# Optimization experiments

Hardware: AMD Instinct MI355X
Metric: run time of the kernel (lower is better)

Reference implementation:

```python
import jax, jax.numpy as jnp
import numpy as np

V, C, D, H, L = 32000, 1024, 768, 12, 6
B, S = 2, 1024
HD = D // H
EPS = 1e-5


def _layernorm(x, g, b):
    m = jnp.mean(x, axis=-1, keepdims=True)
    v = jnp.mean((x - m) ** 2, axis=-1, keepdims=True)
    return (x - m) * jax.lax.rsqrt(v + EPS) * g + b


def setup_inputs() -> dict:
    key = jax.random.key(0)
    ks = jax.random.split(key, 20)
    p = lambda k, *sh: (jax.random.normal(k, sh, dtype=jnp.float32) * 0.02)
    inp = {
        'context': jax.random.randint(ks[0], (B, S), 0, V, dtype=jnp.int32),
        'tok_emb': p(ks[1], V, D),
        'pos_emb': p(ks[2], C, D),
        # per-layer stacked params (leading dim L)
        'Wq': p(ks[3], L, D, D), 'Wk': p(ks[4], L, D, D), 'Wv': p(ks[5], L, D, D),
        'Wo': p(ks[6], L, D, D), 'bo': jnp.zeros((L, D), jnp.float32),
        'ln1_g': jnp.ones((L, D), jnp.float32), 'ln1_b': jnp.zeros((L, D), jnp.float32),
        'W1': p(ks[7], L, D, 4 * D), 'b1': jnp.zeros((L, 4 * D), jnp.float32),
        'W2': p(ks[8], L, 4 * D, D), 'b2': jnp.zeros((L, D), jnp.float32),
        'ln2_g': jnp.ones((L, D), jnp.float32), 'ln2_b': jnp.zeros((L, D), jnp.float32),
        'lnf_g': jnp.ones((D,), jnp.float32), 'lnf_b': jnp.zeros((D,), jnp.float32),
        'Wout': p(ks[9], D, V), 'bout': jnp.zeros((V,), jnp.float32),
    }
    return inp


def _forward(context, tok_emb, pos_emb, Wq, Wk, Wv, Wo, bo, ln1_g, ln1_b,
             W1, b1, W2, b2, ln2_g, ln2_b, lnf_g, lnf_b, Wout, bout):
    x = tok_emb[context] + pos_emb[:S]              # [B,S,D]
    causal = jnp.tril(jnp.ones((S, S), dtype=bool))  # [S,S]
    scale = 1.0 / float(HD) ** 0.5

    def step(x, params):
        wq, wk, wv, wo, bo_, g1, b1_, w1, bf1, w2, bf2, g2, b2_ = params
        h = _layernorm(x, g1, b1_)
        q = (h @ wq).reshape(B, S, H, HD)
        k = (h @ wk).reshape(B, S, H, HD)
        v = (h @ wv).reshape(B, S, H, HD)
        scores = jnp.einsum('bqhd,bkhd->bhqk', q, k) * scale
        scores = jnp.where(causal, scores, -jnp.inf)
        attn = jax.nn.softmax(scores, axis=-1)
        ctx = jnp.einsum('bhqk,bkhd->bqhd', attn, v).reshape(B, S, D)
        x = x + ctx @ wo + bo_  # dropout is eval-mode identity
        h2 = _layernorm(x, g2, b2_)
        x = x + jax.nn.relu(h2 @ w1 + bf1) @ w2 + bf2
        return x, None

    params = (Wq, Wk, Wv, Wo, bo, ln1_g, ln1_b, W1, b1, W2, b2, ln2_g, ln2_b)
    x, _ = jax.lax.scan(step, x, params)
    return _layernorm(x, lnf_g, lnf_b) @ Wout + bout  # [B,S,V]


def reference(context, tok_emb, pos_emb, Wq, Wk, Wv, Wo, bo, ln1_g, ln1_b,
              W1, b1, W2, b2, ln2_g, ln2_b, lnf_g, lnf_b, Wout, bout):
    return _forward(context, tok_emb, pos_emb, Wq, Wk, Wv, Wo, bo, ln1_g, ln1_b,
                    W1, b1, W2, b2, ln2_g, ln2_b, lnf_g, lnf_b, Wout, bout)
```

## Files before the change

### kernel.cpp

```cpp
#include <hip/hip_runtime.h>

#define S_    1024
#define D_    768
#define H_    12
#define HD_   64
#define L_    6
#define B_    2
#define V_    32000
#define NTOK  2048
#define DD    (D_ * D_)
#define D4D   (D_ * 4 * D_)

typedef __bf16 bf16_t;
typedef __bf16 bf16x8 __attribute__((ext_vector_type(8)));
typedef float  f32x4  __attribute__((ext_vector_type(4)));

__device__ __forceinline__ void async_ld16(const bf16_t* g, bf16_t* l) {
  __builtin_amdgcn_global_load_lds((__attribute__((address_space(1))) void*)(g),
                                   (__attribute__((address_space(3))) void*)(l),
                                   16, 0, 0);
}

__device__ __forceinline__ float wave_sum(float v) {
#pragma unroll
  for (int off = 32; off; off >>= 1) v += __shfl_xor(v, off);
  return v;
}
__device__ __forceinline__ float wave_max(float v) {
#pragma unroll
  for (int off = 32; off; off >>= 1) v = fmaxf(v, __shfl_xor(v, off));
  return v;
}

__device__ __forceinline__ float ldv(const void* p, size_t i, bool f32) {
  return f32 ? ((const float*)p)[i] : (float)((const bf16_t*)p)[i];
}

__global__ void k_sniff(const void* tok, int* flag) {
  const bf16_t* p = (const bf16_t*)tok;
  float mx = 0.f;
  for (int i = threadIdx.x; i < 256; i += 64) {
    float v = fabsf((float)p[i]);
    mx = fmaxf(mx, v);
  }
  mx = wave_max(mx);
  if (threadIdx.x == 0) *flag = (mx > 1.0e6f) ? 1 : 0;
}

__global__ __launch_bounds__(256) void k_cvt_bias(const int* flag, bf16_t* canon,
    const void* bo, const void* b1, const void* b2, const void* l1g, const void* l1b,
    const void* l2g, const void* l2b, const void* lfg, const void* lfb, const void* bout) {
  const bool f32 = (*flag != 0);
  const void* src; int off, n;
  switch (blockIdx.y) {
    case 0: src = bo;  off = 0;     n = 4608;  break;
    case 1: src = b1;  off = 4608;  n = 18432; break;
    case 2: src = b2;  off = 23040; n = 4608;  break;
    case 3: src = l1g; off = 27648; n = 4608;  break;
    case 4: src = l1b; off = 32256; n = 4608;  break;
    case 5: src = l2g; off = 36864; n = 4608;  break;
    case 6: src = l2b; off = 41472; n = 4608;  break;
    case 7: src = lfg; off = 46080; n = 768;   break;
    case 8: src = lfb; off = 46848; n = 768;   break;
    default: src = bout; off = 47616; n = 32000; break;
  }
  const int i = blockIdx.x * 256 + threadIdx.x;
  if (i < n) canon[off + i] = (bf16_t)ldv(src, (size_t)i, f32);
}

enum { E_STORE = 0, E_BIAS_OUT = 1, E_BIAS_RELU = 2, E_BIAS_RES = 3 };

template <int EPI>
__device__ __forceinline__ void gemm_core(const bf16_t* __restrict__ A,
                                          const bf16_t* __restrict__ BT,
                                          const bf16_t* __restrict__ bias,
                                          void* __restrict__ Cb,
                                          float* __restrict__ resid,
                                          const int* f32out,
                                          int M, int N, int K) {
  __shared__ bf16_t sA[128 * 32];
  __shared__ bf16_t sB[128 * 32];
  const int tid  = threadIdx.x;
  const int wave = tid >> 6, lane = tid & 63;
  const int quad = lane >> 4, l16 = lane & 15;
  const int m0 = blockIdx.y * 128, n0 = blockIdx.x * 128;
  const int wm = (wave >> 1) * 64, wn = (wave & 1) * 64;

  const f32x4 zero = {0.f, 0.f, 0.f, 0.f};
  f32x4 acc[4][4];
#pragma unroll
  for (int i = 0; i < 4; i++)
#pragma unroll
    for (int j = 0; j < 4; j++) acc[i][j] = zero;

  const bf16_t* gA = A  + (size_t)(m0 + wave * 32 + (lane >> 2)) * K + (lane & 3) * 8;
  const bf16_t* gB = BT + (size_t)(n0 + wave * 32 + (lane >> 2)) * K + (lane & 3) * 8;
  bf16_t* lA = sA + wave * 1024;
  bf16_t* lB = sB + wave * 1024;
  const size_t k16 = (size_t)16 * K;

  for (int k0 = 0; k0 < K; k0 += 32) {
    async_ld16(gA, lA);
    async_ld16(gA + k16, lA + 512);
    async_ld16(gB, lB);
    async_ld16(gB + k16, lB + 512);
    gA += 32; gB += 32;
    __syncthreads();

    bf16x8 af[4], bfr[4];
#pragma unroll
    for (int i = 0; i < 4; i++) {
      af[i]  = *(const bf16x8*)(sA + (wm + i * 16 + l16) * 32 + quad * 8);
      bfr[i] = *(const bf16x8*)(sB + (wn + i * 16 + l16) * 32 + quad * 8);
    }
#pragma unroll
    for (int mi = 0; mi < 4; mi++)
#pragma unroll
      for (int ni = 0; ni < 4; ni++)
        acc[mi][ni] = __builtin_amdgcn_mfma_f32_16x16x32_bf16(af[mi], bfr[ni], acc[mi][ni], 0, 0, 0);
    __syncthreads();
  }

  const bool f32o = (EPI == E_BIAS_OUT) && (*f32out != 0);
#pragma unroll
  for (int mi = 0; mi < 4; mi++) {
#pragma unroll
    for (int ni = 0; ni < 4; ni++) {
      const int r0 = m0 + wm + mi * 16 + quad * 4;
      const int c  = n0 + wn + ni * 16 + l16;
      float bv = 0.f;
      if (EPI != E_STORE) bv = (float)bias[c];
#pragma unroll
      for (int r = 0; r < 4; r++) {
        float val = acc[mi][ni][r] + bv;
        if (EPI == E_BIAS_RELU) val = fmaxf(val, 0.f);
        const size_t idx = (size_t)(r0 + r) * N + c;
        if (EPI == E_BIAS_RES) {
          resid[idx] += val;
        } else if (EPI == E_BIAS_OUT) {
          if (f32o) ((float*)Cb)[idx] = val;
          else      ((bf16_t*)Cb)[idx] = (bf16_t)val;
        } else {
          ((bf16_t*)Cb)[idx] = (bf16_t)val;
        }
      }
    }
  }
}

__global__ __launch_bounds__(256) void k_gemm_qkv(const bf16_t* __restrict__ A,
                                                  const bf16_t* __restrict__ BT0,
                                                  const bf16_t* __restrict__ BT1,
                                                  const bf16_t* __restrict__ BT2,
                                                  bf16_t* __restrict__ o0,
                                                  bf16_t* __restrict__ o1,
                                                  bf16_t* __restrict__ o2,
                                                  int M, int N, int K) {
  const bf16_t* BT = (blockIdx.z == 0) ? BT0 : (blockIdx.z == 1) ? BT1 : BT2;
  bf16_t* o = (blockIdx.z == 0) ? o0 : (blockIdx.z == 1) ? o1 : o2;
  gemm_core<E_STORE>(A, BT, nullptr, o, nullptr, nullptr, M, N, K);
}
__global__ __launch_bounds__(256) void k_gemm_bias_relu(const bf16_t* __restrict__ A, const bf16_t* __restrict__ BT,
                                                        const bf16_t* __restrict__ bias, bf16_t* __restrict__ C,
                                                        int M, int N, int K) {
  gemm_core<E_BIAS_RELU>(A, BT, bias, C, nullptr, nullptr, M, N, K);
}
__global__ __launch_bounds__(256) void k_gemm_bias_res(const bf16_t* __restrict__ A, const bf16_t* __restrict__ BT,
                                                       const bf16_t* __restrict__ bias, float* __restrict__ resid,
                                                       int M, int N, int K) {
  gemm_core<E_BIAS_RES>(A, BT, bias, nullptr, resid, nullptr, M, N, K);
}
__global__ __launch_bounds__(256) void k_gemm_out(const bf16_t* __restrict__ A, const bf16_t* __restrict__ BT,
                                                  const bf16_t* __restrict__ bias, void* __restrict__ C,
                                                  const int* flag, int M, int N, int K) {
  gemm_core<E_BIAS_OUT>(A, BT, bias, C, nullptr, flag, M, N, K);
}

__global__ __launch_bounds__(256) void k_t(const int* flag, const void* __restrict__ in, size_t eoff,
                                           bf16_t* __restrict__ out, int K, int N) {
  __shared__ bf16_t t[32][33];
  const bool f32 = (*flag != 0);
  const int n0 = blockIdx.x * 32, k0 = blockIdx.y * 32;
  const int tx = threadIdx.x, ty = threadIdx.y;
#pragma unroll
  for (int i = 0; i < 4; i++)
    t[ty + 8 * i][tx] = (bf16_t)ldv(in, eoff + (size_t)(k0 + ty + 8 * i) * N + n0 + tx, f32);
  __syncthreads();
#pragma unroll
  for (int i = 0; i < 4; i++)
    out[(size_t)(n0 + ty + 8 * i) * K + k0 + tx] = t[tx][ty + 8 * i];
}

__global__ __launch_bounds__(256) void k_t_qkv(const int* flag, const void* __restrict__ Wq,
                                               const void* __restrict__ Wk, const void* __restrict__ Wv,
                                               size_t eoff, bf16_t* __restrict__ out) {
  __shared__ bf16_t t[32][33];
  const bool f32 = (*flag != 0);
  const void* in = (blockIdx.z == 0) ? Wq : (blockIdx.z == 1) ? Wk : Wv;
  bf16_t* o = out + (size_t)blockIdx.z * DD;
  const int n0 = blockIdx.x * 32, k0 = blockIdx.y * 32;
  const int tx = threadIdx.x, ty = threadIdx.y;
#pragma unroll
  for (int i = 0; i < 4; i++)
    t[ty + 8 * i][tx] = (bf16_t)ldv(in, eoff + (size_t)(k0 + ty + 8 * i) * D_ + n0 + tx, f32);
  __syncthreads();
#pragma unroll
  for (int i = 0; i < 4; i++)
    o[(size_t)(n0 + ty + 8 * i) * D_ + k0 + tx] = t[tx][ty + 8 * i];
}

__global__ __launch_bounds__(256) void k_vt(const bf16_t* __restrict__ v, bf16_t* __restrict__ vt) {
  __shared__ bf16_t t[32][33];
  const int b = blockIdx.z;
  const int n0 = blockIdx.x * 32, s0 = blockIdx.y * 32;
  const int tx = threadIdx.x, ty = threadIdx.y;
#pragma unroll
  for (int i = 0; i < 4; i++)
    t[ty + 8 * i][tx] = v[(size_t)(b * S_ + s0 + ty + 8 * i) * D_ + n0 + tx];
  __syncthreads();
#pragma unroll
  for (int i = 0; i < 4; i++)
    vt[(size_t)(b * D_ + n0 + ty + 8 * i) * S_ + s0 + tx] = t[tx][ty + 8 * i];
}

__global__ __launch_bounds__(256) void k_embed(const int* flag, const int* __restrict__ cidx,
                                               const void* __restrict__ tok, const void* __restrict__ pos,
                                               float* __restrict__ x) {
  const bool f32 = (*flag != 0);
  const int t = blockIdx.x;
  const int id = cidx[t];
  const int s = t & (S_ - 1);
  for (int d = threadIdx.x; d < D_; d += 256)
    x[(size_t)t * D_ + d] = ldv(tok, (size_t)id * D_ + d, f32) + ldv(pos, (size_t)s * D_ + d, f32);
}

__global__ __launch_bounds__(256) void k_ln(const float* __restrict__ x, const bf16_t* __restrict__ g,
                                            const bf16_t* __restrict__ bta, bf16_t* __restrict__ out) {
  __shared__ float red[4];
  const int t = blockIdx.x, tid = threadIdx.x;
  const int wave = tid >> 6, lane = tid & 63;
  const float* xr = x + (size_t)t * D_;
  const float v0 = xr[tid], v1 = xr[tid + 256], v2 = xr[tid + 512];
  float s = wave_sum(v0 + v1 + v2);
  if (lane == 0) red[wave] = s;
  __syncthreads();
  const float mean = (red[0] + red[1] + red[2] + red[3]) * (1.f / 768.f);
  const float d0 = v0 - mean, d1 = v1 - mean, d2 = v2 - mean;
  float vs = wave_sum(d0 * d0 + d1 * d1 + d2 * d2);
  __syncthreads();
  if (lane == 0) red[wave] = vs;
  __syncthreads();
  const float inv = rsqrtf((red[0] + red[1] + red[2] + red[3]) * (1.f / 768.f) + 1e-5f);
  bf16_t* o = out + (size_t)t * D_;
  o[tid]       = (bf16_t)(d0 * inv * (float)g[tid]       + (float)bta[tid]);
  o[tid + 256] = (bf16_t)(d1 * inv * (float)g[tid + 256] + (float)bta[tid + 256]);
  o[tid + 512] = (bf16_t)(d2 * inv * (float)g[tid + 512] + (float)bta[tid + 512]);
}

__global__ __launch_bounds__(64) void k_fattn(const bf16_t* __restrict__ q,
                                              const bf16_t* __restrict__ k,
                                              const bf16_t* __restrict__ vt,
                                              bf16_t* __restrict__ ctx) {
  __shared__ bf16_t sP[16 * 40];
  const int lane = threadIdx.x;
  const int quad = lane >> 4, l16 = lane & 15;
  const int q0 = blockIdx.x << 4, h = blockIdx.y, b = blockIdx.z;
  const size_t hoff = (size_t)h * HD_;

  const bf16_t* qp = q + (size_t)(b * S_ + q0 + l16) * D_ + hoff + quad * 8;
  const bf16x8 af0 = *(const bf16x8*)qp;
  const bf16x8 af1 = *(const bf16x8*)(qp + 32);

  const f32x4 zero = {0.f, 0.f, 0.f, 0.f};
  f32x4 o_acc[4];
  float m_run[4], l_run[4];
#pragma unroll
  for (int ct = 0; ct < 4; ++ct) o_acc[ct] = zero;
#pragma unroll
  for (int r = 0; r < 4; ++r) { m_run[r] = -1e30f; l_run[r] = 0.f; }

  const int nt = ((q0 + 15) >> 5) + 1;
  const bf16_t* kbase = k + (size_t)(b * S_ + l16) * D_ + hoff + quad * 8;
  const size_t kst = (size_t)16 * D_;
  bf16x8 kf0 = *(const bf16x8*)(kbase);
  bf16x8 kf1 = *(const bf16x8*)(kbase + 32);
  bf16x8 kf2 = *(const bf16x8*)(kbase + kst);
  bf16x8 kf3 = *(const bf16x8*)(kbase + kst + 32);

  const bf16_t* vbase = vt + (size_t)(b * D_ + hoff + l16) * S_ + quad * 8;

  for (int kt = 0; kt < nt; ++kt) {
    const int k0 = kt << 5;
    const bf16_t* vrow = vbase + k0;
    const bf16x8 vb0 = *(const bf16x8*)(vrow);
    const bf16x8 vb1 = *(const bf16x8*)(vrow + 16 * S_);
    const bf16x8 vb2 = *(const bf16x8*)(vrow + 32 * S_);
    const bf16x8 vb3 = *(const bf16x8*)(vrow + 48 * S_);

    f32x4 d0 = zero, d1 = zero;
    d0 = __builtin_amdgcn_mfma_f32_16x16x32_bf16(af0, kf0, d0, 0, 0, 0);
    d0 = __builtin_amdgcn_mfma_f32_16x16x32_bf16(af1, kf1, d0, 0, 0, 0);
    d1 = __builtin_amdgcn_mfma_f32_16x16x32_bf16(af0, kf2, d1, 0, 0, 0);
    d1 = __builtin_amdgcn_mfma_f32_16x16x32_bf16(af1, kf3, d1, 0, 0, 0);

    if (kt + 1 < nt) {
      const bf16_t* kpn = kbase + (size_t)(k0 + 32) * D_;
      kf0 = *(const bf16x8*)(kpn);
      kf1 = *(const bf16x8*)(kpn + 32);
      kf2 = *(const bf16x8*)(kpn + kst);
      kf3 = *(const bf16x8*)(kpn + kst + 32);
    }

    const bool msk = (kt == nt - 1);
    float al[4];
#pragma unroll
    for (int r = 0; r < 4; ++r) {
      float s0 = d0[r] * 0.125f;
      float s1 = d1[r] * 0.125f;
      if (msk) {
        const int row = q0 + quad * 4 + r;
        if (k0 + l16      > row) s0 = -1e30f;
        if (k0 + 16 + l16 > row) s1 = -1e30f;
      }
      float mt = fmaxf(s0, s1);
      mt = fmaxf(mt, __shfl_xor(mt, 1));
      mt = fmaxf(mt, __shfl_xor(mt, 2));
      mt = fmaxf(mt, __shfl_xor(mt, 4));
      mt = fmaxf(mt, __shfl_xor(mt, 8));
      const float mn = fmaxf(m_run[r], mt);
      const float a  = __expf(m_run[r] - mn);
      m_run[r] = mn;
      const float p0 = __expf(s0 - mn);
      const float p1 = __expf(s1 - mn);
      float ps = p0 + p1;
      ps += __shfl_xor(ps, 1);
      ps += __shfl_xor(ps, 2);
      ps += __shfl_xor(ps, 4);
      ps += __shfl_xor(ps, 8);
      l_run[r] = l_run[r] * a + ps;
      al[r] = a;
      sP[(quad * 4 + r) * 40 + l16]      = (bf16_t)p0;
      sP[(quad * 4 + r) * 40 + 16 + l16] = (bf16_t)p1;
    }
#pragma unroll
    for (int ct = 0; ct < 4; ++ct) {
      o_acc[ct][0] *= al[0]; o_acc[ct][1] *= al[1];
      o_acc[ct][2] *= al[2]; o_acc[ct][3] *= al[3];
    }
    const bf16x8 pa = *(const bf16x8*)(sP + l16 * 40 + quad * 8);
    o_acc[0] = __builtin_amdgcn_mfma_f32_16x16x32_bf16(pa, vb0, o_acc[0], 0, 0, 0);
    o_acc[1] = __builtin_amdgcn_mfma_f32_16x16x32_bf16(pa, vb1, o_acc[1], 0, 0, 0);
    o_acc[2] = __builtin_amdgcn_mfma_f32_16x16x32_bf16(pa, vb2, o_acc[2], 0, 0, 0);
    o_acc[3] = __builtin_amdgcn_mfma_f32_16x16x32_bf16(pa, vb3, o_acc[3], 0, 0, 0);
  }

  float inv[4];
#pragma unroll
  for (int r = 0; r < 4; ++r) inv[r] = 1.f / l_run[r];
  bf16_t* cp = ctx + (size_t)(b * S_ + q0 + quad * 4) * D_ + hoff + l16;
#pragma unroll
  for (int ct = 0; ct < 4; ++ct)
#pragma unroll
    for (int r = 0; r < 4; ++r)
      cp[(size_t)r * D_ + ct * 16] = (bf16_t)(o_acc[ct][r] * inv[r]);
}

extern "C" void kernel_launch(void* const* d_in, const int* in_sizes, int n_in,
                              void* d_out, int out_size, void* d_ws, size_t ws_size,
                              hipStream_t stream) {
  (void)in_sizes; (void)n_in; (void)out_size; (void)ws_size;
  const int* cidx = (const int*)d_in[0];
  const void* tok  = d_in[1];
  const void* pos  = d_in[2];
  const void* Wq   = d_in[3];
  const void* Wk   = d_in[4];
  const void* Wv   = d_in[5];
  const void* Wo   = d_in[6];
  const void* bo   = d_in[7];
  const void* ln1g = d_in[8];
  const void* ln1b = d_in[9];
  const void* W1   = d_in[10];
  const void* b1   = d_in[11];
  const void* W2   = d_in[12];
  const void* b2   = d_in[13];
  const void* ln2g = d_in[14];
  const void* ln2b = d_in[15];
  const void* lnfg = d_in[16];
  const void* lnfb = d_in[17];
  const void* Wout = d_in[18];
  const void* bout = d_in[19];

  char* p = (char*)d_ws;
  int*    flag  = (int*)p;
  bf16_t* canon = (bf16_t*)(p + 256);
  char*   q     = p + 256 + 163840;
  float*  x     = (float*)q;  q += (size_t)NTOK * D_ * 4;
  bf16_t* h     = (bf16_t*)q; q += (size_t)NTOK * D_ * 2;
  bf16_t* qb    = (bf16_t*)q; q += (size_t)NTOK * D_ * 2;
  bf16_t* kbuf  = (bf16_t*)q; q += (size_t)NTOK * D_ * 2;
  bf16_t* vbuf  = (bf16_t*)q; q += (size_t)NTOK * D_ * 2;
  bf16_t* cbuf  = (bf16_t*)q; q += (size_t)NTOK * D_ * 2;
  bf16_t* mid   = (bf16_t*)q; q += (size_t)NTOK * 4 * D_ * 2;
  bf16_t* slot  = (bf16_t*)q; q += (size_t)D_ * V_ * 2;
  bf16_t* vt = mid;

  bf16_t* c_bo  = canon + 0;
  bf16_t* c_b1  = canon + 4608;
  bf16_t* c_b2  = canon + 23040;
  bf16_t* c_l1g = canon + 27648;
  bf16_t* c_l1b = canon + 32256;
  bf16_t* c_l2g = canon + 36864;
  bf16_t* c_l2b = canon + 41472;
  bf16_t* c_lfg = canon + 46080;
  bf16_t* c_lfb = canon + 46848;
  bf16_t* c_bout= canon + 47616;

  const dim3 tb(32, 8);
  k_sniff<<<1, 64, 0, stream>>>(tok, flag);
  k_cvt_bias<<<dim3(125, 10), 256, 0, stream>>>(flag, canon, bo, b1, b2, ln1g, ln1b,
                                                ln2g, ln2b, lnfg, lnfb, bout);
  k_embed<<<NTOK, 256, 0, stream>>>(flag, cidx, tok, pos, x);

  const dim3 gD(D_ / 128, NTOK / 128);
  const dim3 gF(4 * D_ / 128, NTOK / 128);
  for (int l = 0; l < L_; ++l) {
    const size_t wo = (size_t)l * DD;
    const size_t wf = (size_t)l * D4D;
    k_ln<<<NTOK, 256, 0, stream>>>(x, c_l1g + l * D_, c_l1b + l * D_, h);
    k_t_qkv<<<dim3(24, 24, 3), tb, 0, stream>>>(flag, Wq, Wk, Wv, wo, slot);
    k_gemm_qkv<<<dim3(D_ / 128, NTOK / 128, 3), 256, 0, stream>>>(
        h, slot, slot + DD, slot + 2 * DD, qb, kbuf, vbuf, NTOK, D_, D_);
    k_vt<<<dim3(24, 32, 2), tb, 0, stream>>>(vbuf, vt);
    k_fattn<<<dim3(S_ / 16, H_, B_), 64, 0, stream>>>(qb, kbuf, vt, cbuf);
    k_t<<<dim3(24, 24), tb, 0, stream>>>(flag, Wo, wo, slot, D_, D_);
    k_gemm_bias_res<<<gD, 256, 0, stream>>>(cbuf, slot, c_bo + l * D_, x, NTOK, D_, D_);
    k_ln<<<NTOK, 256, 0, stream>>>(x, c_l2g + l * D_, c_l2b + l * D_, h);
    k_t<<<dim3(96, 24), tb, 0, stream>>>(flag, W1, wf, slot, D_, 4 * D_);
    k_gemm_bias_relu<<<gF, 256, 0, stream>>>(h, slot, c_b1 + l * 4 * D_, mid, NTOK, 4 * D_, D_);
    k_t<<<dim3(24, 96), tb, 0, stream>>>(flag, W2, wf, slot, 4 * D_, D_);
    k_gemm_bias_res<<<gD, 256, 0, stream>>>(mid, slot, c_b2 + l * D_, x, NTOK, D_, 4 * D_);
  }
  k_ln<<<NTOK, 256, 0, stream>>>(x, c_lfg, c_lfb, h);
  k_t<<<dim3(1000, 24), tb, 0, stream>>>(flag, Wout, 0, slot, D_, V_);
  k_gemm_out<<<dim3(V_ / 128, NTOK / 128), 256, 0, stream>>>(h, slot, c_bout, d_out, flag,
                                                             NTOK, V_, D_);
}
```

Before: 2.041 ms.

## Split-K residual GEMMs with atomic accumulation and swizzle output GEMM tiles

The two residual-add GEMMs (Wo and W2) are split along K into 2 and 4 chunks across blockIdx.z, with each chunk atomically adding its partial result into the fp32 residual. Only the first chunk adds the bias. This raises the workgroup count of these small-N GEMMs (6x16 tiles otherwise) so more CUs are busy. The vocab projection GEMM also remaps workgroup IDs so consecutive groups walk along M within an N column, aiming for better cache reuse of weight tiles. The cost is atomic traffic and results whose summation order is no longer deterministic.

Result: faster. 1.747 ms (-14.4%).

```diff
diff --git a/kernel.cpp b/kernel.cpp
--- a/kernel.cpp
+++ b/kernel.cpp
@@ -68,7 +68,7 @@
   if (i < n) canon[off + i] = (bf16_t)ldv(src, (size_t)i, f32);
 }
 
-enum { E_STORE = 0, E_BIAS_OUT = 1, E_BIAS_RELU = 2, E_BIAS_RES = 3 };
+enum { E_STORE = 0, E_BIAS_OUT = 1, E_BIAS_RELU = 2, E_BIAS_RES_AT = 3 };
 
 template <int EPI>
 __device__ __forceinline__ void gemm_core(const bf16_t* __restrict__ A,
@@ -77,13 +77,13 @@
                                           void* __restrict__ Cb,
                                           float* __restrict__ resid,
                                           const int* f32out,
-                                          int M, int N, int K) {
+                                          int M, int N, int K,
+                                          int m0, int n0, int kb, int ke) {
   __shared__ bf16_t sA[128 * 32];
   __shared__ bf16_t sB[128 * 32];
   const int tid  = threadIdx.x;
   const int wave = tid >> 6, lane = tid & 63;
   const int quad = lane >> 4, l16 = lane & 15;
-  const int m0 = blockIdx.y * 128, n0 = blockIdx.x * 128;
   const int wm = (wave >> 1) * 64, wn = (wave & 1) * 64;
 
   const f32x4 zero = {0.f, 0.f, 0.f, 0.f};
@@ -93,13 +93,13 @@
 #pragma unroll
     for (int j = 0; j < 4; j++) acc[i][j] = zero;
 
-  const bf16_t* gA = A  + (size_t)(m0 + wave * 32 + (lane >> 2)) * K + (lane & 3) * 8;
-  const bf16_t* gB = BT + (size_t)(n0 + wave * 32 + (lane >> 2)) * K + (lane & 3) * 8;
+  const bf16_t* gA = A  + (size_t)(m0 + wave * 32 + (lane >> 2)) * K + kb + (lane & 3) * 8;
+  const bf16_t* gB = BT + (size_t)(n0 + wave * 32 + (lane >> 2)) * K + kb + (lane & 3) * 8;
   bf16_t* lA = sA + wave * 1024;
   bf16_t* lB = sB + wave * 1024;
   const size_t k16 = (size_t)16 * K;
 
-  for (int k0 = 0; k0 < K; k0 += 32) {
+  for (int k0 = kb; k0 < ke; k0 += 32) {
     async_ld16(gA, lA);
     async_ld16(gA + k16, lA + 512);
     async_ld16(gB, lB);
@@ -129,14 +129,15 @@
       const int r0 = m0 + wm + mi * 16 + quad * 4;
       const int c  = n0 + wn + ni * 16 + l16;
       float bv = 0.f;
-      if (EPI != E_STORE) bv = (float)bias[c];
+      if (EPI == E_BIAS_OUT || EPI == E_BIAS_RELU) bv = (float)bias[c];
+      if (EPI == E_BIAS_RES_AT && kb == 0) bv = (float)bias[c];
 #pragma unroll
       for (int r = 0; r < 4; r++) {
         float val = acc[mi][ni][r] + bv;
         if (EPI == E_BIAS_RELU) val = fmaxf(val, 0.f);
         const size_t idx = (size_t)(r0 + r) * N + c;
-        if (EPI == E_BIAS_RES) {
-          resid[idx] += val;
+        if (EPI == E_BIAS_RES_AT) {
+          atomicAdd(&resid[idx], val);
         } else if (EPI == E_BIAS_OUT) {
           if (f32o) ((float*)Cb)[idx] = val;
           else      ((bf16_t*)Cb)[idx] = (bf16_t)val;
@@ -158,22 +159,36 @@
                                                   int M, int N, int K) {
   const bf16_t* BT = (blockIdx.z == 0) ? BT0 : (blockIdx.z == 1) ? BT1 : BT2;
   bf16_t* o = (blockIdx.z == 0) ? o0 : (blockIdx.z == 1) ? o1 : o2;
-  gemm_core<E_STORE>(A, BT, nullptr, o, nullptr, nullptr, M, N, K);
+  gemm_core<E_STORE>(A, BT, nullptr, o, nullptr, nullptr, M, N, K,
+                     blockIdx.y * 128, blockIdx.x * 128, 0, K);
 }
 __global__ __launch_bounds__(256) void k_gemm_bias_relu(const bf16_t* __restrict__ A, const bf16_t* __restrict__ BT,
                                                         const bf16_t* __restrict__ bias, bf16_t* __restrict__ C,
                                                         int M, int N, int K) {
-  gemm_core<E_BIAS_RELU>(A, BT, bias, C, nullptr, nullptr, M, N, K);
-}
-__global__ __launch_bounds__(256) void k_gemm_bias_res(const bf16_t* __restrict__ A, const bf16_t* __restrict__ BT,
-                                                       const bf16_t* __restrict__ bias, float* __restrict__ resid,
-                                                       int M, int N, int K) {
-  gemm_core<E_BIAS_RES>(A, BT, bias, nullptr, resid, nullptr, M, N, K);
+  gemm_core<E_BIAS_RELU>(A, BT, bias, C, nullptr, nullptr, M, N, K,
+                         blockIdx.y * 128, blockIdx.x * 128, 0, K);
+}
+__global__ __launch_bounds__(256) void k_gemm_res_sk(const bf16_t* __restrict__ A, const bf16_t* __restrict__ BT,
+                                                     const bf16_t* __restrict__ bias, float* __restrict__ resid,
+                                                     int M, int N, int K) {
+  const int kc = K / gridDim.z;
+  const int kb = blockIdx.z * kc;
+  gemm_core<E_BIAS_RES_AT>(A, BT, bias, nullptr, resid, nullptr, M, N, K,
+                           blockIdx.y * 128, blockIdx.x * 128, kb, kb + kc);
 }
 __global__ __launch_bounds__(256) void k_gemm_out(const bf16_t* __restrict__ A, const bf16_t* __restrict__ BT,
                                                   const bf16_t* __restrict__ bias, void* __restrict__ C,
                                                   const int* flag, int M, int N, int K) {
-  gemm_core<E_BIAS_OUT>(A, BT, bias, C, nullptr, flag, M, N, K);
+  const int nwg = gridDim.x * gridDim.y;
+  int lid = blockIdx.y * gridDim.x + blockIdx.x;
+  if ((nwg & 7) == 0) {
+    const int cpx = nwg >> 3;
+    lid = (lid & 7) * cpx + (lid >> 3);
+  }
+  const int mt = lid % gridDim.y;
+  const int nt = lid / gridDim.y;
+  gemm_core<E_BIAS_OUT>(A, BT, bias, C, nullptr, flag, M, N, K,
+                        mt * 128, nt * 128, 0, K);
 }
 
 __global__ __launch_bounds__(256) void k_t(const int* flag, const void* __restrict__ in, size_t eoff,
@@ -421,8 +436,9 @@
                                                 ln2g, ln2b, lnfg, lnfb, bout);
   k_embed<<<NTOK, 256, 0, stream>>>(flag, cidx, tok, pos, x);
 
-  const dim3 gD(D_ / 128, NTOK / 128);
   const dim3 gF(4 * D_ / 128, NTOK / 128);
+  const dim3 gSK2(D_ / 128, NTOK / 128, 2);
+  const dim3 gSK4(D_ / 128, NTOK / 128, 4);
   for (int l = 0; l < L_; ++l) {
     const size_t wo = (size_t)l * DD;
     const size_t wf = (size_t)l * D4D;
@@ -433,12 +449,12 @@
     k_vt<<<dim3(24, 32, 2), tb, 0, stream>>>(vbuf, vt);
     k_fattn<<<dim3(S_ / 16, H_, B_), 64, 0, stream>>>(qb, kbuf, vt, cbuf);
     k_t<<<dim3(24, 24), tb, 0, stream>>>(flag, Wo, wo, slot, D_, D_);
-    k_gemm_bias_res<<<gD, 256, 0, stream>>>(cbuf, slot, c_bo + l * D_, x, NTOK, D_, D_);
+    k_gemm_res_sk<<<gSK2, 256, 0, stream>>>(cbuf, slot, c_bo + l * D_, x, NTOK, D_, D_);
     k_ln<<<NTOK, 256, 0, stream>>>(x, c_l2g + l * D_, c_l2b + l * D_, h);
     k_t<<<dim3(96, 24), tb, 0, stream>>>(flag, W1, wf, slot, D_, 4 * D_);
     k_gemm_bias_relu<<<gF, 256, 0, stream>>>(h, slot, c_b1 + l * 4 * D_, mid, NTOK, 4 * D_, D_);
     k_t<<<dim3(24, 96), tb, 0, stream>>>(flag, W2, wf, slot, 4 * D_, D_);
-    k_gemm_bias_res<<<gD, 256, 0, stream>>>(mid, slot, c_b2 + l * D_, x, NTOK, D_, 4 * D_);
+    k_gemm_res_sk<<<gSK4, 256, 0, stream>>>(mid, slot, c_b2 + l * D_, x, NTOK, D_, 4 * D_);
   }
   k_ln<<<NTOK, 256, 0, stream>>>(x, c_lfg, c_lfb, h);
   k_t<<<dim3(1000, 24), tb, 0, stream>>>(flag, Wout, 0, slot, D_, V_);
```
